# Optimization experiments

Hardware: AMD Instinct MI355X
Metric: run time of the kernel (lower is better)

Reference implementation:

```python
import jax, jax.numpy as jnp
import numpy as np
from jax import lax

# ---- static config (matches init_kwargs) ----
STRIDE = 16
BASE_SIZE = 16
SCALES = np.array([2., 4., 8., 16., 32.])
RATIOS = np.array([0.5, 1., 2.])
CLIP = 4.14
NMS_THRESH = 0.7
PRE_NMS = 6000
POST_NMS = 300
MIN_SIZE = 16.0


def _whctrs(a):
    w = a[2] - a[0] + 1.0
    h = a[3] - a[1] + 1.0
    return w, h, a[0] + 0.5 * (w - 1.0), a[1] + 0.5 * (h - 1.0)


def _mkanchors(ws, hs, xc, yc):
    return np.stack([xc - 0.5 * (ws - 1.0), yc - 0.5 * (hs - 1.0),
                     xc + 0.5 * (ws - 1.0), yc + 0.5 * (hs - 1.0)], axis=1)


def _base_anchors():
    ba = np.array([1.0, 1.0, BASE_SIZE, BASE_SIZE]) - 1.0
    w, h, xc, yc = _whctrs(ba)
    size = w * h
    ws = np.round(np.sqrt(size / RATIOS))
    hs = np.round(ws * RATIOS)
    ra = _mkanchors(ws, hs, xc, yc)
    out = []
    for i in range(ra.shape[0]):
        w, h, xc, yc = _whctrs(ra[i])
        out.append(_mkanchors(w * SCALES, h * SCALES, xc, yc))
    return np.concatenate(out, axis=0)  # (A,4), A = len(ratios)*len(scales)


def _grid_anchors(Hf, Wf):
    ba = _base_anchors()                       # (A,4)
    sx, sy = np.meshgrid(np.arange(Wf) * STRIDE, np.arange(Hf) * STRIDE)
    shifts = np.stack([sx, sy, sx, sy], axis=-1)          # (Hf,Wf,4)
    anch = shifts[:, :, None, :] + ba[None, None, :, :]    # (Hf,Wf,A,4)
    return jnp.asarray(anch.reshape(1, -1, 4), dtype=jnp.float32)


def _decode_clip(anchors, deltas, img_h, img_w):
    # NormalizedBoxCenterDecoder (stds=1) + clip to image
    aw = anchors[..., 2] - anchors[..., 0]
    ah = anchors[..., 3] - anchors[..., 1]
    ax = anchors[..., 0] + 0.5 * aw
    ay = anchors[..., 1] + 0.5 * ah
    dx, dy, dw, dh = deltas[..., 0], deltas[..., 1], deltas[..., 2], deltas[..., 3]
    ox = dx * aw + ax
    oy = dy * ah + ay
    ow = jnp.exp(jnp.minimum(dw, CLIP)) * aw * 0.5
    oh = jnp.exp(jnp.minimum(dh, CLIP)) * ah * 0.5
    x1 = jnp.clip(ox - ow, 0.0, img_w - 1.0)
    y1 = jnp.clip(oy - oh, 0.0, img_h - 1.0)
    x2 = jnp.clip(ox + ow, 0.0, img_w - 1.0)
    y2 = jnp.clip(oy + oh, 0.0, img_h - 1.0)
    return jnp.stack([x1, y1, x2, y2], axis=-1)


def _nms_single(scores, boxes):
    # scores (N,), boxes (N,4). Greedy NMS, force_suppress, sorted by score desc.
    order = jnp.argsort(-scores)[:PRE_NMS]
    s = scores[order]
    b = boxes[order]
    x1, y1, x2, y2 = b[:, 0], b[:, 1], b[:, 2], b[:, 3]
    area = (x2 - x1) * (y2 - y1)
    iw = jnp.maximum(jnp.minimum(x2[:, None], x2[None, :]) - jnp.maximum(x1[:, None], x1[None, :]), 0.0)
    ih = jnp.maximum(jnp.minimum(y2[:, None], y2[None, :]) - jnp.maximum(y1[:, None], y1[None, :]), 0.0)
    inter = iw * ih
    iou = inter / (area[:, None] + area[None, :] - inter + 1e-12)  # (PRE,PRE)

    supp0 = s < 0.0  # invalid entries (score set to -1 by min_size filter)

    def body(supp, i):
        keep = jnp.logical_not(supp[i])
        new = jnp.where(keep, jnp.logical_or(supp, iou[i] > NMS_THRESH), supp)
        new = new.at[i].set(supp[i])  # never self-suppress
        return new, None

    supp, _ = lax.scan(body, supp0, jnp.arange(PRE_NMS))
    kept = jnp.logical_not(supp)
    perm = jnp.argsort(jnp.where(kept, 0, 1), stable=True)  # kept boxes first, order preserved
    out_s = jnp.where(kept[perm], s[perm], -1.0)
    out_b = jnp.where(kept[perm][:, None], b[perm], -1.0)
    return out_s[:POST_NMS, None], out_b[:POST_NMS]


def _forward(img, x, conv_w, conv_b, score_w, score_b, loc_w, loc_b):
    B, _, Hf, Wf = x.shape
    img_h, img_w = float(img.shape[2]), float(img.shape[3])
    anchors = _grid_anchors(Hf, Wf)  # (1, Hf*Wf*A, 4)

    # conv1 3x3 pad 1 + ReLU
    h = lax.conv_general_dilated(x, conv_w, (1, 1), [(1, 1), (1, 1)],
                                 dimension_numbers=('NCHW', 'OIHW', 'NCHW'))
    h = jax.nn.relu(h + conv_b[None, :, None, None])

    A = score_w.shape[0]
    raw_scores = jnp.einsum('bchw,oc->bhwo', h, score_w.reshape(A, -1)) + score_b
    raw_scores = raw_scores.reshape(B, -1, 1)                       # (B,N,1)
    raw_boxes = jnp.einsum('bchw,oc->bhwo', h, loc_w.reshape(4 * A, -1)) + loc_b
    raw_boxes = raw_boxes.reshape(B, -1, 4)                         # (B,N,4)

    rpn_scores = jax.nn.sigmoid(raw_scores)

    roi = _decode_clip(anchors, raw_boxes, img_h, img_w)            # (B,N,4)
    width = roi[..., 2] - roi[..., 0]
    height = roi[..., 3] - roi[..., 1]
    invalid = jnp.logical_or(width < MIN_SIZE, height < MIN_SIZE)   # (B,N)
    score = jnp.where(invalid[..., None], -1.0, rpn_scores)         # (B,N,1)
    roi = jnp.where(invalid[..., None], -1.0, roi)

    out_s, out_b = jax.vmap(_nms_single)(score[..., 0], roi)        # (B,300,1),(B,300,4)
    return jnp.concatenate([out_s, out_b], axis=-1)                 # (B,300,5)


def setup_inputs() -> dict:
    key = jax.random.key(0)
    ks = jax.random.split(key, 8)
    img = jax.random.normal(ks[0], (1, 3, 1024, 1024), jnp.float32)
    x = jax.random.normal(ks[1], (1, 1024, 64, 64), jnp.float32)
    conv_w = jax.random.normal(ks[2], (1024, 1024, 3, 3), jnp.float32) * 0.01
    conv_b = jnp.zeros((1024,), jnp.float32)
    score_w = jax.random.normal(ks[3], (15, 1024, 1, 1), jnp.float32) * 0.01
    score_b = jnp.zeros((15,), jnp.float32)
    loc_w = jax.random.normal(ks[4], (60, 1024, 1, 1), jnp.float32) * 0.002
    loc_b = jnp.zeros((60,), jnp.float32)
    return {"img": img, "x": x, "conv_w": conv_w, "conv_b": conv_b,
            "score_w": score_w, "score_b": score_b, "loc_w": loc_w, "loc_b": loc_b}


def reference(img, x, conv_w, conv_b, score_w, score_b, loc_w, loc_b):
    return _forward(img, x, conv_w, conv_b, score_w, score_b, loc_w, loc_b)
```

## Files before the change

### kernel.cpp

```cpp
#include <hip/hip_runtime.h>

typedef unsigned int uint;
typedef unsigned short ushort;
typedef unsigned long long u64;

typedef __attribute__((ext_vector_type(8))) short short8;
typedef __attribute__((ext_vector_type(4))) float floatx4;

__device__ inline ushort bf16rne(float v) {
  uint b = __float_as_uint(v);
  uint r = (b + 0x7fffu + ((b >> 16) & 1u)) >> 16;
  return (ushort)r;
}

__device__ inline void gl_lds16(const void* g, void* l) {
  __builtin_amdgcn_global_load_lds(
      (const __attribute__((address_space(1))) unsigned int*)g,
      (__attribute__((address_space(3))) unsigned int*)l, 16, 0, 0);
}


__global__ __launch_bounds__(256) void prep_x(const float* __restrict__ x,
                                              ushort* __restrict__ xh,
                                              ushort* __restrict__ xl) {
  __shared__ float tile[8][512];
  int cc = blockIdx.x, sg = blockIdx.y, t = threadIdx.x;
  int ci0 = cc * 32 + sg * 8;
  size_t obase = (size_t)(cc * 4 + sg) * 4356;
  for (int it = 0; it < 4; ++it) {
    int s0 = blockIdx.z * 2048 + it * 512;
#pragma unroll
    for (int e = 0; e < 8; ++e) {
      tile[e][t] = x[(size_t)(ci0 + e) * 4096 + s0 + t];
      tile[e][t + 256] = x[(size_t)(ci0 + e) * 4096 + s0 + 256 + t];
    }
    __syncthreads();
#pragma unroll
    for (int w = 0; w < 2; ++w) {
      int sl = w * 256 + t;
      int s = s0 + sl;
      int y = s >> 6, xx = s & 63;
      short8 sh, slo;
#pragma unroll
      for (int e = 0; e < 8; ++e) {
        float v = tile[e][sl];
        ushort h2 = bf16rne(v);
        float hf = __uint_as_float((uint)h2 << 16);
        sh[e] = (short)h2;
        slo[e] = (short)bf16rne(v - hf);
      }
      size_t o = (obase + (size_t)(y + 1) * 66 + (xx + 1)) * 8;
      *(short8*)(xh + o) = sh;
      *(short8*)(xl + o) = slo;
    }
    __syncthreads();
  }
}

__global__ __launch_bounds__(256) void prep_w(const float* __restrict__ w,
                                              ushort* __restrict__ wh,
                                              ushort* __restrict__ wl) {
  int cc = blockIdx.x, sg = blockIdx.y, t = threadIdx.x;
  int e = t & 7, col = t >> 3;
  int ci = cc * 32 + sg * 8 + e;
  for (int chunk = 0; chunk < 8; ++chunk) {
    int co = blockIdx.z * 256 + chunk * 32 + col;
    const float* src = w + ((size_t)co * 1024 + ci) * 9;
    float v[9];
#pragma unroll
    for (int o = 0; o < 9; ++o) v[o] = src[o];
#pragma unroll
    for (int off = 0; off < 9; ++off) {
      ushort h2 = bf16rne(v[off]);
      float hf = __uint_as_float((uint)h2 << 16);
      ushort l2 = bf16rne(v[off] - hf);
      size_t oi = ((size_t)(off * 32 + cc) * 4 + sg) * 8192 + (size_t)co * 8 + e;
      wh[oi] = h2;
      wl[oi] = l2;
    }
  }
}

__global__ __launch_bounds__(256) void prep_head(
    const float* __restrict__ score_w, const float* __restrict__ loc_w,
    const float* __restrict__ score_b, const float* __restrict__ loc_b,
    ushort* __restrict__ wh, ushort* __restrict__ wl, float* __restrict__ bh) {
  int idx = blockIdx.x * 256 + threadIdx.x;
  int o = idx >> 10, ci = idx & 1023;
  float v = 0.f;
  if (o < 15) v = score_w[o * 1024 + ci];
  else if (o < 75) v = loc_w[(o - 15) * 1024 + ci];
  ushort h2 = bf16rne(v);
  float hf = __uint_as_float((uint)h2 << 16);
  int cc = ci >> 5, sg = (ci >> 3) & 3, e = ci & 7;
  size_t oi = ((size_t)(cc * 4 + sg) * 128 + o) * 8 + e;
  wh[oi] = h2;
  wl[oi] = bf16rne(v - hf);
  if (idx < 128) bh[idx] = (idx < 15) ? score_b[idx] : ((idx < 75) ? loc_b[idx - 15] : 0.f);
}

__global__ __launch_bounds__(256, 1) void gemm_conv(
    const ushort* __restrict__ Ahi, const ushort* __restrict__ Alo,
    const ushort* __restrict__ Bhi, const ushort* __restrict__ Blo,
    const float* __restrict__ bias, ushort* __restrict__ outHi,
    ushort* __restrict__ outLo) {
  constexpr int NC = 288;
  constexpr int ASEC = 128 * 32;
  constexpr int BSEC = 64 * 32;
  constexpr int BUFU = 2 * ASEC + 2 * BSEC;
  __shared__ ushort sm[2 * BUFU];
  const int t = threadIdx.x;
  const int m0 = blockIdx.x * 128;
  const int n0 = blockIdx.y * 64;

  const int lane = t & 63, wv = t >> 6;
  const int wm = (wv & 1) * 64, wn = (wv >> 1) * 32;
  const int rA = wm + (lane & 15);
  const int rB = wn + (lane & 15);
  const int segA = (lane >> 4) * 2048;
  const int segB = (lane >> 4) * 1024;

  auto stage = [&](int c, int bufIdx) {
    ushort* secAh = sm + bufIdx * BUFU;
    ushort* secAl = secAh + ASEC;
    ushort* secBh = secAl + ASEC;
    ushort* secBl = secBh + BSEC;
    int off = c >> 5, cc = c & 31;
    int oy = off / 3, ox = off - 3 * oy;
#pragma unroll
    for (int q = 0; q < 2; ++q) {
      int L = t + 256 * q;
      int row = L & 127, seg = L >> 7;
      int m = m0 + row, y = m >> 6, xq = m & 63;
      size_t aoff = ((size_t)(cc * 4 + seg) * 4356 + (y + oy) * 66 + (xq + ox)) * 16;
      gl_lds16((const char*)Ahi + aoff, (char*)secAh + L * 16);
      gl_lds16((const char*)Alo + aoff, (char*)secAl + L * 16);
    }
    {
      int L = t;
      int row = L & 63, seg = L >> 6;
      size_t boff = (((size_t)(off * 32 + cc) * 4 + seg) * 1024 + (n0 + row)) * 16;
      gl_lds16((const char*)Bhi + boff, (char*)secBh + L * 16);
      gl_lds16((const char*)Blo + boff, (char*)secBl + L * 16);
    }
  };

  floatx4 acc[4][2];
#pragma unroll
  for (int i = 0; i < 4; ++i)
#pragma unroll
    for (int j = 0; j < 2; ++j) acc[i][j] = (floatx4){0.f, 0.f, 0.f, 0.f};

  auto compute = [&](const ushort* sb) {
    const char* cAh = (const char*)sb;
    const char* cAl = (const char*)(sb + ASEC);
    const char* cBh = (const char*)(sb + 2 * ASEC);
    const char* cBl = (const char*)(sb + 2 * ASEC + BSEC);
    short8 ah[4], al[4], bh2[2], bl2[2];
#pragma unroll
    for (int i = 0; i < 4; ++i) {
      int pa = segA + (rA + 16 * i) * 16;
      ah[i] = *(const short8*)(cAh + pa);
      al[i] = *(const short8*)(cAl + pa);
    }
#pragma unroll
    for (int j = 0; j < 2; ++j) {
      int pb = segB + (rB + 16 * j) * 16;
      bh2[j] = *(const short8*)(cBh + pb);
      bl2[j] = *(const short8*)(cBl + pb);
    }
#pragma unroll
    for (int i = 0; i < 4; ++i)
#pragma unroll
      for (int j = 0; j < 2; ++j) {
        acc[i][j] = __builtin_amdgcn_mfma_f32_16x16x32_bf16(ah[i], bh2[j], acc[i][j], 0, 0, 0);
        acc[i][j] = __builtin_amdgcn_mfma_f32_16x16x32_bf16(ah[i], bl2[j], acc[i][j], 0, 0, 0);
        acc[i][j] = __builtin_amdgcn_mfma_f32_16x16x32_bf16(al[i], bh2[j], acc[i][j], 0, 0, 0);
      }
  };

  stage(0, 0);
  for (int kc = 0; kc < NC; ++kc) {
    __syncthreads();
    if (kc + 1 < NC) stage(kc + 1, (kc + 1) & 1);
    compute(sm + (kc & 1) * BUFU);
  }

#pragma unroll
  for (int i = 0; i < 4; ++i)
#pragma unroll
    for (int j = 0; j < 2; ++j) {
      int nn = n0 + wn + 16 * j + (lane & 15);
      float bv = bias[nn];
#pragma unroll
      for (int r = 0; r < 4; ++r) {
        int mm = m0 + wm + 16 * i + (lane >> 4) * 4 + r;
        float v = fmaxf(acc[i][j][r] + bv, 0.f);
        ushort h2 = bf16rne(v);
        float hf = __uint_as_float((uint)h2 << 16);
        ushort l2 = bf16rne(v - hf);
        int cc = nn >> 5, sg = (nn >> 3) & 3, e = nn & 7;
        size_t ho = ((size_t)(cc * 4 + sg) * 4096 + mm) * 8 + e;
        outHi[ho] = h2;
        outLo[ho] = l2;
      }
    }
}

__global__ __launch_bounds__(256, 1) void gemm_head_decode(
    const ushort* __restrict__ Ahi, const ushort* __restrict__ Alo,
    const ushort* __restrict__ Bhi, const ushort* __restrict__ Blo,
    const float* __restrict__ bias, float* __restrict__ scores,
    float4* __restrict__ boxes, uint* __restrict__ key32,
    uint* __restrict__ hist) {
  constexpr int BM = 32, BN = 128, NCH = 32;
  constexpr int ASEC = BM * 32;
  constexpr int BUFU = 2 * ASEC;
  constexpr int MI = 2, NJ = 2;
  __shared__ ushort sm[2 * BUFU];
  __shared__ float rawT[32][128];
  const int t = threadIdx.x;
  const int m0 = blockIdx.x * BM;

  const int lane = t & 63, wv = t >> 6;
  const int wn = wv * 32;
  const int rA = lane & 15;
  const int segA = (lane >> 4) * (BM * 16);

  auto stage = [&](int c, int bufIdx) {
    ushort* secAh = sm + bufIdx * BUFU;
    ushort* secAl = secAh + ASEC;
    for (int L = t; L < BM * 4; L += 256) {
      int row = L % BM, seg = L / BM;
      size_t aoff = ((size_t)(c * 4 + seg) * 4096 + (m0 + row)) * 16;
      gl_lds16((const char*)Ahi + aoff, (char*)secAh + L * 16);
      gl_lds16((const char*)Alo + aoff, (char*)secAl + L * 16);
    }
  };

  auto loadB = [&](int c, short8* bh, short8* bl) {
    int sg = lane >> 4;
#pragma unroll
    for (int j = 0; j < NJ; ++j) {
      int co = wn + (lane & 15) + 16 * j;
      size_t boff = (((size_t)(c * 4 + sg)) * 128 + co) * 16;
      bh[j] = *(const short8*)((const char*)Bhi + boff);
      bl[j] = *(const short8*)((const char*)Blo + boff);
    }
  };

  floatx4 acc[MI][NJ];
#pragma unroll
  for (int i = 0; i < MI; ++i)
#pragma unroll
    for (int j = 0; j < NJ; ++j) acc[i][j] = (floatx4){0.f, 0.f, 0.f, 0.f};

  auto compute = [&](const ushort* sb, const short8* bh2, const short8* bl2) {
    const char* cAh = (const char*)sb;
    const char* cAl = (const char*)(sb + ASEC);
    short8 ah[MI], al[MI];
#pragma unroll
    for (int i = 0; i < MI; ++i) {
      int pa = segA + (rA + 16 * i) * 16;
      ah[i] = *(const short8*)(cAh + pa);
      al[i] = *(const short8*)(cAl + pa);
    }
#pragma unroll
    for (int i = 0; i < MI; ++i)
#pragma unroll
      for (int j = 0; j < NJ; ++j) {
        acc[i][j] = __builtin_amdgcn_mfma_f32_16x16x32_bf16(ah[i], bh2[j], acc[i][j], 0, 0, 0);
        acc[i][j] = __builtin_amdgcn_mfma_f32_16x16x32_bf16(ah[i], bl2[j], acc[i][j], 0, 0, 0);
        acc[i][j] = __builtin_amdgcn_mfma_f32_16x16x32_bf16(al[i], bh2[j], acc[i][j], 0, 0, 0);
      }
  };

  short8 b0h[NJ], b0l[NJ], b1h[NJ], b1l[NJ];
  stage(0, 0);
  loadB(0, b0h, b0l);
  for (int kc = 0; kc < NCH; kc += 2) {
    __syncthreads();
    if (kc + 1 < NCH) { stage(kc + 1, 1); loadB(kc + 1, b1h, b1l); }
    compute(sm, b0h, b0l);
    __syncthreads();
    if (kc + 2 < NCH) { stage(kc + 2, 0); loadB(kc + 2, b0h, b0l); }
    compute(sm + BUFU, b1h, b1l);
  }

  __syncthreads();
#pragma unroll
  for (int i = 0; i < MI; ++i)
#pragma unroll
    for (int j = 0; j < NJ; ++j) {
      int nn = wn + 16 * j + (lane & 15);
      float bv = bias[nn];
#pragma unroll
      for (int r = 0; r < 4; ++r) {
        int lm = 16 * i + (lane >> 4) * 4 + r;
        rawT[lm][nn] = acc[i][j][r] + bv;
      }
    }
  __syncthreads();

#pragma unroll
  for (int it = 0; it < 2; ++it) {
    int item = it * 256 + t;
    if (item >= 480) break;
    int lm = item / 15, a = item - lm * 15;
    int m = m0 + lm;
    int i = m * 15 + a;
    int y = m >> 6, x = m & 63;
    const float* rp = &rawT[lm][0];
    float logit = rp[a];
    float dx = rp[15 + 4 * a], dy = rp[16 + 4 * a];
    float dw = rp[17 + 4 * a], dh = rp[18 + 4 * a];
    int rr = a / 5, ss = a - rr * 5;
    float sc5 = (float)(2 << ss);
    float W = ((rr == 0) ? 23.f : (rr == 1) ? 16.f : 11.f) * sc5;
    float H = ((rr == 0) ? 12.f : (rr == 1) ? 16.f : 22.f) * sc5;
    float aw = W - 1.f, ah = H - 1.f;
    float ax = x * 16.f + 7.5f, ay = y * 16.f + 7.5f;
    float ox = dx * aw + ax, oyc = dy * ah + ay;
    float ow = expf(fminf(dw, 4.14f)) * aw * 0.5f;
    float oh = expf(fminf(dh, 4.14f)) * ah * 0.5f;
    float x1 = fminf(fmaxf(ox - ow, 0.f), 1023.f);
    float y1 = fminf(fmaxf(oyc - oh, 0.f), 1023.f);
    float x2 = fminf(fmaxf(ox + ow, 0.f), 1023.f);
    float y2 = fminf(fmaxf(oyc + oh, 0.f), 1023.f);
    bool inval = ((x2 - x1) < 16.f) || ((y2 - y1) < 16.f);
    float sc = inval ? -1.f : (1.f / (1.f + expf(-logit)));
    scores[i] = sc;
    boxes[i] = inval ? make_float4(-1.f, -1.f, -1.f, -1.f) : make_float4(x1, y1, x2, y2);
    uint kb = __float_as_uint(sc);
    uint key = (kb & 0x80000000u) ? ~kb : (kb | 0x80000000u);
    key32[i] = key;
    atomicAdd(&hist[key >> 16], 1u);
  }
}

__global__ __launch_bounds__(256) void seg_sum(const uint* __restrict__ hist,
                                               uint* __restrict__ segsum) {
  __shared__ uint red[256];
  int b = blockIdx.x, t = threadIdx.x;
  red[t] = hist[b * 256 + t];
  __syncthreads();
  for (int d = 128; d > 0; d >>= 1) {
    if (t < d) red[t] += red[t + d];
    __syncthreads();
  }
  if (t == 0) segsum[b] = red[0];
}

__global__ __launch_bounds__(256) void find_t16(const uint* __restrict__ hist,
                                                const uint* __restrict__ segsum,
                                                uint* __restrict__ selT) {
  __shared__ uint ps[256];
  __shared__ int segS;
  int t = threadIdx.x;
  ps[t] = segsum[t];
  __syncthreads();
  for (int d = 1; d < 256; d <<= 1) {
    uint v = ps[t] + ((t + d < 256) ? ps[t + d] : 0u);
    __syncthreads();
    ps[t] = v;
    __syncthreads();
  }
  if (ps[t] >= 6000u && (t == 255 || ps[t + 1] < 6000u)) segS = t;
  __syncthreads();
  int sg = segS;
  uint base = (sg == 255) ? 0u : ps[sg + 1];
  uint h2 = hist[sg * 256 + t];
  __syncthreads();
  ps[t] = h2;
  __syncthreads();
  for (int d = 1; d < 256; d <<= 1) {
    uint v = ps[t] + ((t + d < 256) ? ps[t + d] : 0u);
    __syncthreads();
    ps[t] = v;
    __syncthreads();
  }
  if (base + ps[t] >= 6000u && (t == 255 || base + ps[t + 1] < 6000u))
    *selT = (uint)(sg * 256 + t);
}

__global__ __launch_bounds__(256) void gather_k(const uint* __restrict__ key32,
                                                const uint* __restrict__ selT,
                                                uint* __restrict__ cnt,
                                                u64* __restrict__ cand) {
  int i = blockIdx.x * 256 + threadIdx.x;
  uint T = *selT;
  uint k = key32[i];
  if ((k >> 16) >= T) {
    uint pos = atomicAdd(cnt, 1u);
    if (pos < 8192) cand[pos] = ((u64)k << 32) | (u64)(~(uint)i);
  }
}

__global__ __launch_bounds__(1024) void sort_gather(
    const u64* __restrict__ cand, const uint* __restrict__ cnt,
    const float* __restrict__ scores, const float4* __restrict__ boxes,
    float* __restrict__ sortedS, float4* __restrict__ sortedB) {
  extern __shared__ u64 sk[];
  int t = threadIdx.x;
  int C = (int)*cnt;
  if (C > 8192) C = 8192;
  for (int j = t; j < 8192; j += 1024) sk[j] = (j < C) ? cand[j] : 0ull;
  __syncthreads();
  for (int k = 2; k <= 8192; k <<= 1) {
    for (int j2 = k >> 1; j2 > 0; j2 >>= 1) {
      for (int p = t; p < 4096; p += 1024) {
        int i = ((p & ~(j2 - 1)) << 1) | (p & (j2 - 1));
        int ix = i | j2;
        u64 a = sk[i], b = sk[ix];
        bool ddir = (i & k) != 0;
        if ((a < b) != ddir) { sk[i] = b; sk[ix] = a; }
      }
      __syncthreads();
    }
  }
  for (int j = t; j < 6016; j += 1024) {
    if (j < 6000) {
      u64 key = sk[j];
      uint idx = ~(uint)(key & 0xffffffffu);
      sortedS[j] = scores[idx];
      sortedB[j] = boxes[idx];
    } else {
      sortedS[j] = -1.f;
      sortedB[j] = make_float4(0.f, 0.f, 0.f, 0.f);
    }
  }
}

__global__ __launch_bounds__(64) void iou_mask(const float4* __restrict__ boxes,
                                               u64* __restrict__ mask) {
  __shared__ float cx1[64], cy1[64], cx2[64], cy2[64], car[64];
  int bi = blockIdx.x, bj = blockIdx.y, t = threadIdx.x;
  float4 cb = boxes[bj * 64 + t];
  cx1[t] = cb.x; cy1[t] = cb.y; cx2[t] = cb.z; cy2[t] = cb.w;
  car[t] = (cb.z - cb.x) * (cb.w - cb.y);
  __syncthreads();
  int r = bi * 64 + t;
  float4 rb = boxes[r];
  float ra = (rb.z - rb.x) * (rb.w - rb.y);
  u64 wd = 0;
#pragma unroll 8
  for (int j = 0; j < 64; ++j) {
    float iw = fmaxf(fminf(rb.z, cx2[j]) - fmaxf(rb.x, cx1[j]), 0.f);
    float ih = fmaxf(fminf(rb.w, cy2[j]) - fmaxf(rb.y, cy1[j]), 0.f);
    float inter = iw * ih;
    float iou = inter / (ra + car[j] - inter + 1e-12f);
    if (iou > 0.7f && r != bj * 64 + j) wd |= (1ull << j);
  }
  mask[(size_t)r * 128 + bj] = wd;
}

__global__ __launch_bounds__(64) void nms_scan(const u64* __restrict__ mask,
                                               const float* __restrict__ sortedS,
                                               const float4* __restrict__ sortedB,
                                               float* __restrict__ out) {
  __shared__ int klist[300];
  int lane = threadIdx.x;
  u64 Sx = 0, Sy = 0;
  for (int w2 = 0; w2 < 94; ++w2) {
    bool neg = sortedS[w2 * 64 + lane] < 0.f;
    u64 m2 = __ballot(neg);
    if ((w2 >> 1) == lane) { if (w2 & 1) Sy = m2; else Sx = m2; }
  }
  int count = 0;
  for (int w2 = 0; w2 < 94 && count < 300; ++w2) {
    u64 cur = __shfl((w2 & 1) ? Sy : Sx, w2 >> 1);
    u64 rem = ~cur;
    if (w2 == 93) rem &= (1ull << 48) - 1;
    if (!rem) continue;
    u64 W = 0;
    if ((rem >> lane) & 1)
      W = mask[(size_t)(w2 * 64 + lane) * 128 + w2];
    u64 acc = 0, live = rem;
    bool full = false;
    while (live) {
      int b = __builtin_ctzll(live);
      acc |= 1ull << b;
      ++count;
      if (count == 300) { full = true; break; }
      u64 wb = __shfl(W, b);
      live &= ~wb;
      live &= (b == 63) ? 0ull : (~0ull << (b + 1));
    }
    if (lane == 0) {
      u64 a2 = acc;
      int idx = count - __builtin_popcountll(acc);
      while (a2) {
        int b = __builtin_ctzll(a2);
        klist[idx++] = w2 * 64 + b;
        a2 &= a2 - 1;
      }
    }
    if (full) break;
    u64 a2 = acc;
    int r0 = -1, r1 = -1, r2 = -1, r3 = -1;
    ulonglong2 v0, v1, v2, v3;
    if (a2) { int b = __builtin_ctzll(a2); a2 &= a2 - 1; r0 = w2 * 64 + b;
      v0 = ((const ulonglong2*)(mask + (size_t)r0 * 128))[lane]; }
    if (a2) { int b = __builtin_ctzll(a2); a2 &= a2 - 1; r1 = w2 * 64 + b;
      v1 = ((const ulonglong2*)(mask + (size_t)r1 * 128))[lane]; }
    if (a2) { int b = __builtin_ctzll(a2); a2 &= a2 - 1; r2 = w2 * 64 + b;
      v2 = ((const ulonglong2*)(mask + (size_t)r2 * 128))[lane]; }
    if (a2) { int b = __builtin_ctzll(a2); a2 &= a2 - 1; r3 = w2 * 64 + b;
      v3 = ((const ulonglong2*)(mask + (size_t)r3 * 128))[lane]; }
    while (r0 >= 0) {
      Sx |= v0.x;
      Sy |= v0.y;
      r0 = r1; v0 = v1;
      r1 = r2; v1 = v2;
      r2 = r3; v2 = v3;
      r3 = -1;
      if (a2) { int b = __builtin_ctzll(a2); a2 &= a2 - 1; r3 = w2 * 64 + b;
        v3 = ((const ulonglong2*)(mask + (size_t)r3 * 128))[lane]; }
    }
  }
  __syncthreads();
  for (int j = lane; j < 300; j += 64) {
    float s;
    float4 bb;
    if (j < count) {
      int i = klist[j];
      s = sortedS[i];
      bb = sortedB[i];
    } else {
      s = -1.f;
      bb = make_float4(-1.f, -1.f, -1.f, -1.f);
    }
    out[j * 5 + 0] = s;
    out[j * 5 + 1] = bb.x;
    out[j * 5 + 2] = bb.y;
    out[j * 5 + 3] = bb.z;
    out[j * 5 + 4] = bb.w;
  }
}

constexpr size_t O_XH = 0;
constexpr size_t O_XL = 8921088;
constexpr size_t O_WTH = 17842176;
constexpr size_t O_WTL = 36716544;
constexpr size_t O_HH = 55590912;
constexpr size_t O_HL = 63979520;
constexpr size_t O_WHH = 72368128;
constexpr size_t O_WHL = 72630272;
constexpr size_t O_BHD = 72892416;
constexpr size_t O_SC = 72892928;
constexpr size_t O_BX = 73138688;
constexpr size_t O_KEY = 74121728;
constexpr size_t O_HIST = 74367488;
constexpr size_t O_CNT = 74629632;
constexpr size_t O_CAND = 74629888;
constexpr size_t O_SELT = 74695424;
constexpr size_t O_SS = 74695680;
constexpr size_t O_SB = 74719744;
constexpr size_t O_MASK = 17842176;
constexpr size_t O_SEG = 24002560;

extern "C" void kernel_launch(void* const* d_in, const int* in_sizes, int n_in,
                              void* d_out, int out_size, void* d_ws,
                              size_t ws_size, hipStream_t stream) {
  (void)in_sizes; (void)n_in; (void)out_size; (void)ws_size;
  const float* x = (const float*)d_in[1];
  const float* conv_w = (const float*)d_in[2];
  const float* conv_b = (const float*)d_in[3];
  const float* score_w = (const float*)d_in[4];
  const float* score_b = (const float*)d_in[5];
  const float* loc_w = (const float*)d_in[6];
  const float* loc_b = (const float*)d_in[7];
  float* out = (float*)d_out;
  char* ws = (char*)d_ws;

  ushort* xh = (ushort*)(ws + O_XH);
  ushort* xl = (ushort*)(ws + O_XL);
  ushort* wTh = (ushort*)(ws + O_WTH);
  ushort* wTl = (ushort*)(ws + O_WTL);
  ushort* hh = (ushort*)(ws + O_HH);
  ushort* hl = (ushort*)(ws + O_HL);
  ushort* wHh = (ushort*)(ws + O_WHH);
  ushort* wHl = (ushort*)(ws + O_WHL);
  float* biasH = (float*)(ws + O_BHD);
  float* scores = (float*)(ws + O_SC);
  float4* boxes = (float4*)(ws + O_BX);
  uint* key32 = (uint*)(ws + O_KEY);
  uint* hist = (uint*)(ws + O_HIST);
  uint* cnt = (uint*)(ws + O_CNT);
  u64* cand = (u64*)(ws + O_CAND);
  uint* selT = (uint*)(ws + O_SELT);
  float* sortedS = (float*)(ws + O_SS);
  float4* sortedB = (float4*)(ws + O_SB);
  u64* mask = (u64*)(ws + O_MASK);
  uint* segsum = (uint*)(ws + O_SEG);

  hipMemsetAsync(ws + O_XH, 0, 2 * 8921088, stream);
  hipMemsetAsync(ws + O_HIST, 0, 262144 + 256, stream);

  prep_x<<<dim3(32, 4, 2), 256, 0, stream>>>(x, xh, xl);
  prep_w<<<dim3(32, 4, 4), 256, 0, stream>>>(conv_w, wTh, wTl);
  prep_head<<<512, 256, 0, stream>>>(score_w, loc_w, score_b, loc_b, wHh, wHl, biasH);

  gemm_conv<<<dim3(32, 16), 256, 0, stream>>>(xh, xl, wTh, wTl, conv_b, hh, hl);
  gemm_head_decode<<<dim3(128, 1), 256, 0, stream>>>(hh, hl, wHh, wHl, biasH,
                                                     scores, boxes, key32, hist);

  seg_sum<<<256, 256, 0, stream>>>(hist, segsum);
  find_t16<<<1, 256, 0, stream>>>(hist, segsum, selT);
  gather_k<<<240, 256, 0, stream>>>(key32, selT, cnt, cand);
  sort_gather<<<1, 1024, 65536, stream>>>(cand, cnt, scores, boxes, sortedS, sortedB);
  iou_mask<<<dim3(94, 94), 64, 0, stream>>>(sortedB, mask);
  nms_scan<<<1, 64, 0, stream>>>(mask, sortedS, sortedB, out);
}
```

Before: 699.5 us.

## Merge prep kernels and top-k selection kernels, drop memsets

Combines the x, conv-weight and head-weight prep kernels into one launch, which also zeroes only the padding border of the packed input and clears the histogram, replacing two large memsets. The histogram reduction, threshold search, candidate gather and bitonic sort are fused into a single 1024-thread block that uses shared-memory atomics instead of global ones. The aim is to cut launch count and memset traffic. The cost is that the gather and reduction now run on one block only, serialising the scan of 61k keys.

```diff
diff --git a/kernel.cpp b/kernel.cpp
--- a/kernel.cpp
+++ b/kernel.cpp
@@ -20,83 +20,97 @@
 }
 
 
-__global__ __launch_bounds__(256) void prep_x(const float* __restrict__ x,
-                                              ushort* __restrict__ xh,
-                                              ushort* __restrict__ xl) {
-  __shared__ float tile[8][512];
-  int cc = blockIdx.x, sg = blockIdx.y, t = threadIdx.x;
-  int ci0 = cc * 32 + sg * 8;
-  size_t obase = (size_t)(cc * 4 + sg) * 4356;
-  for (int it = 0; it < 4; ++it) {
-    int s0 = blockIdx.z * 2048 + it * 512;
-#pragma unroll
-    for (int e = 0; e < 8; ++e) {
-      tile[e][t] = x[(size_t)(ci0 + e) * 4096 + s0 + t];
-      tile[e][t + 256] = x[(size_t)(ci0 + e) * 4096 + s0 + 256 + t];
-    }
-    __syncthreads();
-#pragma unroll
-    for (int w = 0; w < 2; ++w) {
-      int sl = w * 256 + t;
-      int s = s0 + sl;
-      int y = s >> 6, xx = s & 63;
-      short8 sh, slo;
-#pragma unroll
-      for (int e = 0; e < 8; ++e) {
-        float v = tile[e][sl];
-        ushort h2 = bf16rne(v);
-        float hf = __uint_as_float((uint)h2 << 16);
-        sh[e] = (short)h2;
-        slo[e] = (short)bf16rne(v - hf);
-      }
-      size_t o = (obase + (size_t)(y + 1) * 66 + (xx + 1)) * 8;
-      *(short8*)(xh + o) = sh;
-      *(short8*)(xl + o) = slo;
-    }
-    __syncthreads();
-  }
-}
-
-__global__ __launch_bounds__(256) void prep_w(const float* __restrict__ w,
-                                              ushort* __restrict__ wh,
-                                              ushort* __restrict__ wl) {
-  int cc = blockIdx.x, sg = blockIdx.y, t = threadIdx.x;
-  int e = t & 7, col = t >> 3;
-  int ci = cc * 32 + sg * 8 + e;
-  for (int chunk = 0; chunk < 8; ++chunk) {
-    int co = blockIdx.z * 256 + chunk * 32 + col;
-    const float* src = w + ((size_t)co * 1024 + ci) * 9;
-    float v[9];
-#pragma unroll
-    for (int o = 0; o < 9; ++o) v[o] = src[o];
-#pragma unroll
-    for (int off = 0; off < 9; ++off) {
-      ushort h2 = bf16rne(v[off]);
-      float hf = __uint_as_float((uint)h2 << 16);
-      ushort l2 = bf16rne(v[off] - hf);
-      size_t oi = ((size_t)(off * 32 + cc) * 4 + sg) * 8192 + (size_t)co * 8 + e;
-      wh[oi] = h2;
-      wl[oi] = l2;
-    }
-  }
-}
-
-__global__ __launch_bounds__(256) void prep_head(
+__global__ __launch_bounds__(256) void prep_all(
+    const float* __restrict__ x, const float* __restrict__ conv_w,
     const float* __restrict__ score_w, const float* __restrict__ loc_w,
     const float* __restrict__ score_b, const float* __restrict__ loc_b,
-    ushort* __restrict__ wh, ushort* __restrict__ wl, float* __restrict__ bh) {
-  int idx = blockIdx.x * 256 + threadIdx.x;
-  int o = idx >> 10, ci = idx & 1023;
-  float v = 0.f;
-  if (o < 15) v = score_w[o * 1024 + ci];
-  else if (o < 75) v = loc_w[(o - 15) * 1024 + ci];
-  ushort h2 = bf16rne(v);
-  float hf = __uint_as_float((uint)h2 << 16);
-  int cc = ci >> 5, sg = (ci >> 3) & 3, e = ci & 7;
-  size_t oi = ((size_t)(cc * 4 + sg) * 128 + o) * 8 + e;
-  wh[oi] = h2;
-  wl[oi] = bf16rne(v - hf);
-  if (idx < 128) bh[idx] = (idx < 15) ? score_b[idx] : ((idx < 75) ? loc_b[idx - 15] : 0.f);
+    ushort* __restrict__ xh, ushort* __restrict__ xl,
+    ushort* __restrict__ wTh, ushort* __restrict__ wTl,
+    ushort* __restrict__ wHh, ushort* __restrict__ wHl,
+    float* __restrict__ biasH, uint* __restrict__ hist) {
+  __shared__ float tile[8][512];
+  const int b = blockIdx.x, t = threadIdx.x;
+  if (b < 256) {
+    int cc = b >> 3, sg = (b >> 1) & 3, z = b & 1;
+    int ci0 = cc * 32 + sg * 8;
+    size_t obase = (size_t)(cc * 4 + sg) * 4356;
+    if (z == 0) {
+      short8 z8 = {};
+      for (int k = t; k < 260; k += 256) {
+        int s;
+        if (k < 66) s = k;
+        else if (k < 132) s = 65 * 66 + (k - 66);
+        else if (k < 196) s = (k - 131) * 66;
+        else s = (k - 195) * 66 + 65;
+        size_t o = (obase + s) * 8;
+        *(short8*)(xh + o) = z8;
+        *(short8*)(xl + o) = z8;
+      }
+    }
+    for (int it = 0; it < 4; ++it) {
+      int s0 = z * 2048 + it * 512;
+#pragma unroll
+      for (int e = 0; e < 8; ++e) {
+        tile[e][t] = x[(size_t)(ci0 + e) * 4096 + s0 + t];
+        tile[e][t + 256] = x[(size_t)(ci0 + e) * 4096 + s0 + 256 + t];
+      }
+      __syncthreads();
+#pragma unroll
+      for (int w = 0; w < 2; ++w) {
+        int sl = w * 256 + t;
+        int s = s0 + sl;
+        int y = s >> 6, xx = s & 63;
+        short8 sh, slo;
+#pragma unroll
+        for (int e = 0; e < 8; ++e) {
+          float v = tile[e][sl];
+          ushort h2 = bf16rne(v);
+          float hf = __uint_as_float((uint)h2 << 16);
+          sh[e] = (short)h2;
+          slo[e] = (short)bf16rne(v - hf);
+        }
+        size_t o = (obase + (size_t)(y + 1) * 66 + (xx + 1)) * 8;
+        *(short8*)(xh + o) = sh;
+        *(short8*)(xl + o) = slo;
+      }
+      __syncthreads();
+    }
+  } else if (b < 768) {
+    int q = b - 256;
+    int cc = q >> 4, sg = (q >> 2) & 3, zz = q & 3;
+    int e = t & 7, col = t >> 3;
+    int ci = cc * 32 + sg * 8 + e;
+    for (int chunk = 0; chunk < 8; ++chunk) {
+      int co = zz * 256 + chunk * 32 + col;
+      const float* src = conv_w + ((size_t)co * 1024 + ci) * 9;
+      float v[9];
+#pragma unroll
+      for (int o = 0; o < 9; ++o) v[o] = src[o];
+#pragma unroll
+      for (int off = 0; off < 9; ++off) {
+        ushort h2 = bf16rne(v[off]);
+        float hf = __uint_as_float((uint)h2 << 16);
+        ushort l2 = bf16rne(v[off] - hf);
+        size_t oi = ((size_t)(off * 32 + cc) * 4 + sg) * 8192 + (size_t)co * 8 + e;
+        wTh[oi] = h2;
+        wTl[oi] = l2;
+      }
+    }
+  } else {
+    int idx = (b - 768) * 256 + t;
+    int o = idx >> 10, ci = idx & 1023;
+    float v = 0.f;
+    if (o < 15) v = score_w[o * 1024 + ci];
+    else if (o < 75) v = loc_w[(o - 15) * 1024 + ci];
+    ushort h2 = bf16rne(v);
+    float hf = __uint_as_float((uint)h2 << 16);
+    int cc = ci >> 5, sg = (ci >> 3) & 3, e = ci & 7;
+    size_t oi = ((size_t)(cc * 4 + sg) * 128 + o) * 8 + e;
+    wHh[oi] = h2;
+    wHl[oi] = bf16rne(v - hf);
+    if (idx < 128) biasH[idx] = (idx < 15) ? score_b[idx] : ((idx < 75) ? loc_b[idx - 15] : 0.f);
+    if (idx < 65536) hist[idx] = 0u;
+  }
 }
 
 __global__ __launch_bounds__(256, 1) void gemm_conv(
@@ -338,82 +352,75 @@
   }
 }
 
-__global__ __launch_bounds__(256) void seg_sum(const uint* __restrict__ hist,
-                                               uint* __restrict__ segsum) {
-  __shared__ uint red[256];
-  int b = blockIdx.x, t = threadIdx.x;
-  red[t] = hist[b * 256 + t];
-  __syncthreads();
-  for (int d = 128; d > 0; d >>= 1) {
-    if (t < d) red[t] += red[t + d];
-    __syncthreads();
-  }
-  if (t == 0) segsum[b] = red[0];
-}
-
-__global__ __launch_bounds__(256) void find_t16(const uint* __restrict__ hist,
-                                                const uint* __restrict__ segsum,
-                                                uint* __restrict__ selT) {
+__global__ __launch_bounds__(1024) void topk(
+    const uint* __restrict__ hist, const uint* __restrict__ key32,
+    const float* __restrict__ scores, const float4* __restrict__ boxes,
+    float* __restrict__ sortedS, float4* __restrict__ sortedB) {
+  __shared__ u64 sk[8192];
+  __shared__ uint p4[1024];
   __shared__ uint ps[256];
   __shared__ int segS;
-  int t = threadIdx.x;
-  ps[t] = segsum[t];
+  __shared__ uint selT, cntL;
+  const int t = threadIdx.x;
+  uint s = 0;
+  const uint4* h4 = (const uint4*)(hist + t * 64);
+#pragma unroll 4
+  for (int i = 0; i < 16; ++i) {
+    uint4 v = h4[i];
+    s += v.x + v.y + v.z + v.w;
+  }
+  p4[t] = s;
+  if (t == 0) cntL = 0;
+  __syncthreads();
+  if (t < 256) ps[t] = p4[4 * t] + p4[4 * t + 1] + p4[4 * t + 2] + p4[4 * t + 3];
   __syncthreads();
   for (int d = 1; d < 256; d <<= 1) {
-    uint v = ps[t] + ((t + d < 256) ? ps[t + d] : 0u);
+    uint v = 0;
+    if (t < 256) v = ps[t] + ((t + d < 256) ? ps[t + d] : 0u);
     __syncthreads();
-    ps[t] = v;
+    if (t < 256) ps[t] = v;
     __syncthreads();
   }
-  if (ps[t] >= 6000u && (t == 255 || ps[t + 1] < 6000u)) segS = t;
+  if (t < 256 && ps[t] >= 6000u && (t == 255 || ps[t + 1] < 6000u)) segS = t;
   __syncthreads();
   int sg = segS;
   uint base = (sg == 255) ? 0u : ps[sg + 1];
-  uint h2 = hist[sg * 256 + t];
-  __syncthreads();
-  ps[t] = h2;
+  uint h2 = (t < 256) ? hist[sg * 256 + t] : 0u;
+  __syncthreads();
+  if (t < 256) ps[t] = h2;
   __syncthreads();
   for (int d = 1; d < 256; d <<= 1) {
-    uint v = ps[t] + ((t + d < 256) ? ps[t + d] : 0u);
+    uint v = 0;
+    if (t < 256) v = ps[t] + ((t + d < 256) ? ps[t + d] : 0u);
     __syncthreads();
-    ps[t] = v;
+    if (t < 256) ps[t] = v;
     __syncthreads();
   }
-  if (base + ps[t] >= 6000u && (t == 255 || base + ps[t + 1] < 6000u))
-    *selT = (uint)(sg * 256 + t);
-}
-
-__global__ __launch_bounds__(256) void gather_k(const uint* __restrict__ key32,
-                                                const uint* __restrict__ selT,
-                                                uint* __restrict__ cnt,
-                                                u64* __restrict__ cand) {
-  int i = blockIdx.x * 256 + threadIdx.x;
-  uint T = *selT;
-  uint k = key32[i];
-  if ((k >> 16) >= T) {
-    uint pos = atomicAdd(cnt, 1u);
-    if (pos < 8192) cand[pos] = ((u64)k << 32) | (u64)(~(uint)i);
-  }
-}
-
-__global__ __launch_bounds__(1024) void sort_gather(
-    const u64* __restrict__ cand, const uint* __restrict__ cnt,
-    const float* __restrict__ scores, const float4* __restrict__ boxes,
-    float* __restrict__ sortedS, float4* __restrict__ sortedB) {
-  extern __shared__ u64 sk[];
-  int t = threadIdx.x;
-  int C = (int)*cnt;
+  if (t < 256 && base + ps[t] >= 6000u && (t == 255 || base + ps[t + 1] < 6000u))
+    selT = (uint)(sg * 256 + t);
+  __syncthreads();
+  uint T = selT;
+  for (int j = 0; j < 60; ++j) {
+    int i = j * 1024 + t;
+    uint k = key32[i];
+    if ((k >> 16) >= T) {
+      uint pos = atomicAdd(&cntL, 1u);
+      if (pos < 8192) sk[pos] = ((u64)k << 32) | (u64)(~(uint)i);
+    }
+  }
+  __syncthreads();
+  int C = (int)cntL;
   if (C > 8192) C = 8192;
-  for (int j = t; j < 8192; j += 1024) sk[j] = (j < C) ? cand[j] : 0ull;
+  for (int j = C + t; j < 8192; j += 1024) sk[j] = 0ull;
   __syncthreads();
   for (int k = 2; k <= 8192; k <<= 1) {
     for (int j2 = k >> 1; j2 > 0; j2 >>= 1) {
       for (int p = t; p < 4096; p += 1024) {
         int i = ((p & ~(j2 - 1)) << 1) | (p & (j2 - 1));
         int ix = i | j2;
-        u64 a = sk[i], b = sk[ix];
+        u64 a = sk[i], b2 = sk[ix];
         bool ddir = (i & k) != 0;
-        if ((a < b) != ddir) { sk[i] = b; sk[ix] = a; }
+        if ((a < b2) != ddir) { sk[i] = b2; sk[ix] = a; }
       }
       __syncthreads();
     }
@@ -551,13 +558,9 @@
 constexpr size_t O_BX = 73138688;
 constexpr size_t O_KEY = 74121728;
 constexpr size_t O_HIST = 74367488;
-constexpr size_t O_CNT = 74629632;
-constexpr size_t O_CAND = 74629888;
-constexpr size_t O_SELT = 74695424;
 constexpr size_t O_SS = 74695680;
 constexpr size_t O_SB = 74719744;
 constexpr size_t O_MASK = 17842176;
-constexpr size_t O_SEG = 24002560;
 
 extern "C" void kernel_launch(void* const* d_in, const int* in_sizes, int n_in,
                               void* d_out, int out_size, void* d_ws,
@@ -586,29 +589,16 @@
   float4* boxes = (float4*)(ws + O_BX);
   uint* key32 = (uint*)(ws + O_KEY);
   uint* hist = (uint*)(ws + O_HIST);
-  uint* cnt = (uint*)(ws + O_CNT);
-  u64* cand = (u64*)(ws + O_CAND);
-  uint* selT = (uint*)(ws + O_SELT);
   float* sortedS = (float*)(ws + O_SS);
   float4* sortedB = (float4*)(ws + O_SB);
   u64* mask = (u64*)(ws + O_MASK);
-  uint* segsum = (uint*)(ws + O_SEG);
-
-  hipMemsetAsync(ws + O_XH, 0, 2 * 8921088, stream);
-  hipMemsetAsync(ws + O_HIST, 0, 262144 + 256, stream);
-
-  prep_x<<<dim3(32, 4, 2), 256, 0, stream>>>(x, xh, xl);
-  prep_w<<<dim3(32, 4, 4), 256, 0, stream>>>(conv_w, wTh, wTl);
-  prep_head<<<512, 256, 0, stream>>>(score_w, loc_w, score_b, loc_b, wHh, wHl, biasH);
-
+
+  prep_all<<<1280, 256, 0, stream>>>(x, conv_w, score_w, loc_w, score_b, loc_b,
+                                     xh, xl, wTh, wTl, wHh, wHl, biasH, hist);
   gemm_conv<<<dim3(32, 16), 256, 0, stream>>>(xh, xl, wTh, wTl, conv_b, hh, hl);
   gemm_head_decode<<<dim3(128, 1), 256, 0, stream>>>(hh, hl, wHh, wHl, biasH,
                                                      scores, boxes, key32, hist);
-
-  seg_sum<<<256, 256, 0, stream>>>(hist, segsum);
-  find_t16<<<1, 256, 0, stream>>>(hist, segsum, selT);
-  gather_k<<<240, 256, 0, stream>>>(key32, selT, cnt, cand);
-  sort_gather<<<1, 1024, 65536, stream>>>(cand, cnt, scores, boxes, sortedS, sortedB);
+  topk<<<1, 1024, 0, stream>>>(hist, key32, scores, boxes, sortedS, sortedB);
   iou_mask<<<dim3(94, 94), 64, 0, stream>>>(sortedB, mask);
   nms_scan<<<1, 64, 0, stream>>>(mask, sortedS, sortedB, out);
 }
```

Result: no change. 694.1 us (-0.8%).
